# Performance work log

Measured on AMD Instinct MI355X. Metric: run time of the kernel, lower is better.

## Reference

```python
import jax, jax.numpy as jnp
import numpy as np

EPS = 1e-5
N_GROUPS = 32
N_HEAD = 1


def group_norm(x, gamma, beta):
    B, C, H, W = x.shape
    xg = x.reshape(B, N_GROUPS, C // N_GROUPS, H, W)
    mean = xg.mean(axis=(2, 3, 4), keepdims=True)
    var = xg.var(axis=(2, 3, 4), keepdims=True)
    xg = (xg - mean) * jax.lax.rsqrt(var + EPS)
    x = xg.reshape(B, C, H, W)
    return x * gamma[None, :, None, None] + beta[None, :, None, None]


def setup_inputs() -> dict:
    key = jax.random.key(0)
    k1, k2, k3 = jax.random.split(key, 3)
    B, C, H, W = 32, 512, 32, 32
    x = jax.random.normal(k1, (B, C, H, W), dtype=jnp.float32)
    gamma = jnp.ones((C,), dtype=jnp.float32)
    beta = jnp.zeros((C,), dtype=jnp.float32)
    # fan_avg uniform init for 1x1 convs (bound = sqrt(3*scale/fan_avg))
    bound_qkv = np.sqrt(3.0 / ((C + 3 * C) / 2))
    w_qkv = jax.random.uniform(k2, (3 * C, C), dtype=jnp.float32,
                               minval=-bound_qkv, maxval=bound_qkv)
    b_qkv = jnp.zeros((3 * C,), dtype=jnp.float32)
    bound_out = np.sqrt(3.0 * 1e-10 / C)
    w_out = jax.random.uniform(k3, (C, C), dtype=jnp.float32,
                               minval=-bound_out, maxval=bound_out)
    b_out = jnp.zeros((C,), dtype=jnp.float32)
    return {"x": x, "gamma": gamma, "beta": beta,
            "w_qkv": w_qkv, "b_qkv": b_qkv, "w_out": w_out, "b_out": b_out}


def reference(x, gamma, beta, w_qkv, b_qkv, w_out, b_out):
    B, C, H, W = x.shape
    n_head = N_HEAD
    head_dim = C // n_head
    norm = group_norm(x, gamma, beta)
    # 1x1 conv == channel matmul: [B,3C,H,W]
    qkv = jnp.einsum('bchw,oc->bohw', norm, w_qkv) + b_qkv[None, :, None, None]
    qkv = qkv.reshape(B, n_head, 3 * head_dim, H, W)
    q, k, v = jnp.split(qkv, 3, axis=2)  # each [B,n,hd,H,W]
    scale = 1.0 / np.sqrt(head_dim)
    attn = jnp.einsum('bnchw,bncyx->bnhwyx', q, k) * scale
    attn = jax.nn.softmax(attn.reshape(B, n_head, H, W, H * W), axis=-1)
    attn = attn.reshape(B, n_head, H, W, H, W)
    out = jnp.einsum('bnhwyx,bncyx->bnchw', attn, v).reshape(B, C, H, W)
    out = jnp.einsum('bchw,oc->bohw', out, w_out) + b_out[None, :, None, None]
    return out + x
```

## Files before the change

kernel.cpp:

```cpp
#include <hip/hip_runtime.h>
#include <hip/hip_bf16.h>

#define B_    32
#define C_    512
#define S_    1024
#define G_    32
#define CPG_  16
#define EPS_  1e-5f
#define SCALE_ 0.044194173824159216f

typedef __attribute__((ext_vector_type(4))) float  floatx4;
typedef __attribute__((ext_vector_type(8))) __bf16 bf16x8;

__device__ __forceinline__ float bf2f(unsigned short u) {
    union { unsigned int i; float f; } v; v.i = ((unsigned int)u) << 16; return v.f;
}
__device__ __forceinline__ unsigned short f2bf(float f) {
    union { float f; unsigned int i; } v; v.f = f;
    unsigned int r = v.i + 0x7fffu + ((v.i >> 16) & 1u);
    return (unsigned short)(r >> 16);
}

__device__ __forceinline__ void gl16(const unsigned short* g, unsigned short* l) {
    __builtin_amdgcn_global_load_lds(
        (const __attribute__((address_space(1))) unsigned int*)g,
        (__attribute__((address_space(3))) unsigned int*)l, 16, 0, 0);
}

__global__ __launch_bounds__(256) void gn_stats(const float* __restrict__ x,
                                                float2* __restrict__ stats,
                                                float* __restrict__ lbuf) {
    if (threadIdx.x < 8)
        ((float4*)lbuf)[blockIdx.x * 8 + threadIdx.x] = make_float4(0.f, 0.f, 0.f, 0.f);
    const size_t base = (size_t)blockIdx.x * (CPG_ * S_);
    const float4* xp = (const float4*)(x + base);
    float s = 0.f, ss = 0.f;
    for (int i = threadIdx.x; i < (CPG_ * S_) / 4; i += 256) {
        float4 v = xp[i];
        s  += v.x + v.y + v.z + v.w;
        ss += v.x * v.x + v.y * v.y + v.z * v.z + v.w * v.w;
    }
    #pragma unroll
    for (int o = 32; o; o >>= 1) { s += __shfl_down(s, o); ss += __shfl_down(ss, o); }
    __shared__ float a1[4], a2[4];
    const int wid = threadIdx.x >> 6, lane = threadIdx.x & 63;
    if (lane == 0) { a1[wid] = s; a2[wid] = ss; }
    __syncthreads();
    if (threadIdx.x == 0) {
        float S  = a1[0] + a1[1] + a1[2] + a1[3];
        float SS = a2[0] + a2[1] + a2[2] + a2[3];
        float mean = S * (1.f / 16384.f);
        float var  = SS * (1.f / 16384.f) - mean * mean;
        stats[blockIdx.x] = make_float2(mean, rsqrtf(var + EPS_));
    }
}

__global__ __launch_bounds__(256) void tcast(const float* __restrict__ w,
                                             const float* __restrict__ w_out,
                                             unsigned short* __restrict__ WqT,
                                             unsigned short* __restrict__ WkT,
                                             unsigned short* __restrict__ WvT,
                                             unsigned short* __restrict__ Woutb) {
    const int z = blockIdx.z;
    const int m0 = blockIdx.y * 64, c0 = blockIdx.x * 64;
    const int t = threadIdx.x, tr = t >> 4, tc4 = (t & 15) * 4;
    if (z == 3) {
        #pragma unroll
        for (int i = 0; i < 4; i++) {
            int r = tr + i * 16;
            float4 v = *(const float4*)(w_out + (size_t)(m0 + r) * 512 + c0 + tc4);
            ushort4 o4;
            o4.x = f2bf(v.x); o4.y = f2bf(v.y); o4.z = f2bf(v.z); o4.w = f2bf(v.w);
            *(ushort4*)(Woutb + (size_t)(m0 + r) * 512 + c0 + tc4) = o4;
        }
        return;
    }
    const float* src = w + (size_t)z * 262144;
    unsigned short* dst = (z == 0) ? WqT : (z == 1) ? WkT : WvT;
    __shared__ float tile[64][65];
    #pragma unroll
    for (int i = 0; i < 4; i++) {
        int r = tr + i * 16;
        float4 v = *(const float4*)(src + (size_t)(m0 + r) * 512 + c0 + tc4);
        tile[r][tc4 + 0] = v.x; tile[r][tc4 + 1] = v.y;
        tile[r][tc4 + 2] = v.z; tile[r][tc4 + 3] = v.w;
    }
    __syncthreads();
    #pragma unroll
    for (int i = 0; i < 4; i++) {
        int sr = tr + i * 16;
        ushort4 o4;
        o4.x = f2bf(tile[tc4 + 0][sr]); o4.y = f2bf(tile[tc4 + 1][sr]);
        o4.z = f2bf(tile[tc4 + 2][sr]); o4.w = f2bf(tile[tc4 + 3][sr]);
        *(ushort4*)(dst + (size_t)(c0 + sr) * 512 + m0 + tc4) = o4;
    }
}

__global__ __launch_bounds__(256) void vecprep(const unsigned short* __restrict__ WkT,
                                               const float* __restrict__ w_out,
                                               const float* __restrict__ b_qkv,
                                               float* __restrict__ bzv) {
    const int o = blockIdx.x, t = threadIdx.x;
    float us = 0.f, bv = 0.f;
    #pragma unroll
    for (int mm = 0; mm < 2; mm++) {
        int m = t + mm * 256;
        us += b_qkv[m] * bf2f(WkT[(size_t)o * 512 + m]);
        bv += w_out[(size_t)o * 512 + m] * b_qkv[1024 + m];
    }
    #pragma unroll
    for (int sh = 32; sh; sh >>= 1) { us += __shfl_down(us, sh); bv += __shfl_down(bv, sh); }
    __shared__ float a[2][4];
    const int wid = t >> 6, lane = t & 63;
    if (lane == 0) { a[0][wid] = us; a[1][wid] = bv; }
    __syncthreads();
    if (t == 0) {
        bzv[o]       = (a[0][0] + a[0][1] + a[0][2] + a[0][3]) * SCALE_;
        bzv[512 + o] =  a[1][0] + a[1][1] + a[1][2] + a[1][3];
    }
}

template<bool SWAP>
__device__ __forceinline__ void mfma_loop(const unsigned short* __restrict__ Ag, int lda,
                                          const unsigned short* __restrict__ Bg, int ldb,
                                          int K, int m0, int n0,
                                          unsigned short* ldsA, unsigned short* ldsB,
                                          floatx4 (&acc)[4][4]) {
    const int t = threadIdx.x, lane = t & 63, wave = t >> 6;
    const int wr = (wave >> 1) * 64, wc = (wave & 1) * 64;
    const int lrow = lane & 15, lq = lane >> 4;
    const int srow = wave * 16 + (lane >> 2);
    const int scol = (lane & 3) * 8;
    const unsigned short* gA0 = Ag + (size_t)(m0 + srow) * lda + scol;
    const unsigned short* gA1 = gA0 + (size_t)64 * lda;
    const unsigned short* gB0 = Bg + (size_t)(n0 + srow) * ldb + scol;
    const unsigned short* gB1 = gB0 + (size_t)64 * ldb;
    unsigned short* lA = ldsA + wave * 512;
    unsigned short* lB = ldsB + wave * 512;
    for (int k0 = 0; k0 < K; k0 += 64) {
        gl16(gA0 + k0,      lA);
        gl16(gA1 + k0,      lA + 2048);
        gl16(gA0 + k0 + 32, lA + 4096);
        gl16(gA1 + k0 + 32, lA + 6144);
        gl16(gB0 + k0,      lB);
        gl16(gB1 + k0,      lB + 2048);
        gl16(gB0 + k0 + 32, lB + 4096);
        gl16(gB1 + k0 + 32, lB + 6144);
        __syncthreads();
        #pragma unroll
        for (int sub = 0; sub < 2; sub++) {
            bf16x8 af[4], bfr[4];
            #pragma unroll
            for (int i = 0; i < 4; i++) {
                af[i]  = *(const bf16x8*)(ldsA + sub * 4096 + (wr + i * 16 + lrow) * 32 + lq * 8);
                bfr[i] = *(const bf16x8*)(ldsB + sub * 4096 + (wc + i * 16 + lrow) * 32 + lq * 8);
            }
            #pragma unroll
            for (int i = 0; i < 4; i++)
                #pragma unroll
                for (int j = 0; j < 4; j++) {
                    if (SWAP)
                        acc[i][j] = __builtin_amdgcn_mfma_f32_16x16x32_bf16(bfr[j], af[i], acc[i][j], 0, 0, 0);
                    else
                        acc[i][j] = __builtin_amdgcn_mfma_f32_16x16x32_bf16(af[i], bfr[j], acc[i][j], 0, 0, 0);
                }
        }
        __syncthreads();
    }
}

__global__ __launch_bounds__(256) void prep_gemm(const unsigned short* __restrict__ WkT,
                                                 const unsigned short* __restrict__ WqT,
                                                 const unsigned short* __restrict__ Woutb,
                                                 const unsigned short* __restrict__ WvT,
                                                 unsigned short* __restrict__ Wzv) {
    __shared__ __align__(16) unsigned short ldsA[2 * 128 * 32];
    __shared__ __align__(16) unsigned short ldsB[2 * 128 * 32];
    const int z = blockIdx.z;
    const int m0 = blockIdx.y * 128, n0 = blockIdx.x * 128;
    const int t = threadIdx.x, lane = t & 63, wave = t >> 6;
    const int wr = (wave >> 1) * 64, wc = (wave & 1) * 64;
    const int lrow = lane & 15, lq = lane >> 4;
    floatx4 acc[4][4];
    #pragma unroll
    for (int i = 0; i < 4; i++)
        #pragma unroll
        for (int j = 0; j < 4; j++) acc[i][j] = (floatx4){0.f, 0.f, 0.f, 0.f};
    const unsigned short* Ag = z ? Woutb : WkT;
    const unsigned short* Bg = z ? WvT   : WqT;
    mfma_loop<true>(Ag, 512, Bg, 512, 512, m0, n0, ldsA, ldsB, acc);
    const float sc = z ? 1.f : SCALE_;
    #pragma unroll
    for (int i = 0; i < 4; i++)
        #pragma unroll
        for (int j = 0; j < 4; j++) {
            int row = z * 512 + m0 + wr + i * 16 + lrow;
            int col = n0 + wc + j * 16 + lq * 4;
            floatx4 v = acc[i][j];
            ushort4 o4;
            o4.x = f2bf(v[0] * sc); o4.y = f2bf(v[1] * sc);
            o4.z = f2bf(v[2] * sc); o4.w = f2bf(v[3] * sc);
            *(ushort4*)(Wzv + (size_t)row * 512 + col) = o4;
        }
}

__global__ __launch_bounds__(256) void xnt_kernel(const float* __restrict__ x,
                                                  const float* __restrict__ gamma,
                                                  const float* __restrict__ beta,
                                                  const float2* __restrict__ stats,
                                                  unsigned short* __restrict__ xnt) {
    const int b = blockIdx.z, c0 = blockIdx.y * 64, s0 = blockIdx.x * 64;
    __shared__ float tile[64][65];
    const float* xb = x + (size_t)b * (C_ * S_);
    const int t = threadIdx.x, tr = t >> 4, tc4 = (t & 15) * 4;
    #pragma unroll
    for (int i = 0; i < 4; i++) {
        int r = tr + i * 16;
        int c = c0 + r;
        float2 mv = stats[b * G_ + (c >> 4)];
        float a  = mv.y * gamma[c];
        float bb = beta[c] - mv.x * a;
        float4 v = *(const float4*)(xb + (size_t)c * S_ + s0 + tc4);
        tile[r][tc4 + 0] = a * v.x + bb;
        tile[r][tc4 + 1] = a * v.y + bb;
        tile[r][tc4 + 2] = a * v.z + bb;
        tile[r][tc4 + 3] = a * v.w + bb;
    }
    __syncthreads();
    unsigned short* xo = xnt + (size_t)b * (S_ * C_);
    #pragma unroll
    for (int i = 0; i < 4; i++) {
        int sr = tr + i * 16;
        ushort4 o4;
        o4.x = f2bf(tile[tc4 + 0][sr]);
        o4.y = f2bf(tile[tc4 + 1][sr]);
        o4.z = f2bf(tile[tc4 + 2][sr]);
        o4.w = f2bf(tile[tc4 + 3][sr]);
        *(ushort4*)(xo + (size_t)(s0 + sr) * C_ + c0 + tc4) = o4;
    }
}

template<bool SWAP>
__device__ __forceinline__ void mfma256_loop(const unsigned short* __restrict__ Ag, int lda,
                                             const unsigned short* __restrict__ Bg, int ldb,
                                             int nt, int m0, int n0,
                                             unsigned short* lds, floatx4 (&acc)[8][4]) {
    const int tid  = threadIdx.x;
    const int lane = tid & 63, wave = tid >> 6;
    const int wm = wave >> 2, wn = wave & 3;
    const int lrow = lane & 15, lq = lane >> 4;
    const int cs = lq ^ ((lrow >> 1) & 3);

    int aofs[8], bofs[4];
    #pragma unroll
    for (int i = 0; i < 8; i++) aofs[i] = (wm * 128 + i * 16 + lrow) * 32 + cs * 8;
    #pragma unroll
    for (int j = 0; j < 4; j++) bofs[j] = (wn * 64 + j * 16 + lrow) * 32 + cs * 8;

    const int sr  = tid >> 2;
    const int scs = (tid & 3) ^ ((tid >> 3) & 3);
    const unsigned short* gA = Ag + (size_t)(m0 + sr) * lda + scs * 8;
    const unsigned short* gB = Bg + (size_t)(n0 + sr) * ldb + scs * 8;
    const size_t a128 = (size_t)128 * lda, b128 = (size_t)128 * ldb;
    unsigned short* lwA = lds + wave * 512;
    unsigned short* lwB = lds + 32768 + wave * 512;

#define STAGE_A(t, kh) do { \
    unsigned short* lb_ = lwA + ((t) & 1) * 16384 + (kh) * 8192; \
    const unsigned short* gp_ = gA + (t) * 64 + (kh) * 32; \
    gl16(gp_, lb_); gl16(gp_ + a128, lb_ + 4096); } while (0)
#define STAGE_B(t, kh) do { \
    unsigned short* lb_ = lwB + ((t) & 1) * 16384 + (kh) * 8192; \
    const unsigned short* gp_ = gB + (t) * 64 + (kh) * 32; \
    gl16(gp_, lb_); gl16(gp_ + b128, lb_ + 4096); } while (0)

    STAGE_A(0, 0); STAGE_B(0, 0); STAGE_A(0, 1); STAGE_B(0, 1);
    STAGE_A(1, 0); STAGE_B(1, 0);
    asm volatile("s_waitcnt vmcnt(4)" ::: "memory");
    __builtin_amdgcn_s_barrier();

    bf16x8 af[4], bfr[4];
    for (int u = 0; u < nt; ++u) {
        const int p = u & 1;
        #pragma unroll
        for (int ph = 0; ph < 4; ++ph) {
            const int kh = ph >> 1, mh = ph & 1;
            const int slab = p * 16384 + kh * 8192;
            if (mh == 0) {
                #pragma unroll
                for (int j = 0; j < 4; j++)
                    bfr[j] = *(const bf16x8*)(lds + 32768 + slab + bofs[j]);
            }
            #pragma unroll
            for (int i = 0; i < 4; i++)
                af[i] = *(const bf16x8*)(lds + slab + aofs[mh * 4 + i]);
            if (ph == 0)      { if (u + 1 < nt) STAGE_A(u + 1, 1); }
            else if (ph == 1) { if (u + 1 < nt) STAGE_B(u + 1, 1); }
            else if (ph == 2) { if (u + 2 < nt) STAGE_A(u + 2, 0); }
            else              { if (u + 2 < nt) STAGE_B(u + 2, 0); }
            __builtin_amdgcn_s_barrier();
            asm volatile("s_waitcnt lgkmcnt(0)" ::: "memory");
            __builtin_amdgcn_sched_barrier(0);
            __builtin_amdgcn_s_setprio(1);
            #pragma unroll
            for (int i = 0; i < 4; i++)
                #pragma unroll
                for (int j = 0; j < 4; j++) {
                    if (SWAP)
                        acc[mh * 4 + i][j] = __builtin_amdgcn_mfma_f32_16x16x32_bf16(
                            bfr[j], af[i], acc[mh * 4 + i][j], 0, 0, 0);
                    else
                        acc[mh * 4 + i][j] = __builtin_amdgcn_mfma_f32_16x16x32_bf16(
                            af[i], bfr[j], acc[mh * 4 + i][j], 0, 0, 0);
                }
            __builtin_amdgcn_s_setprio(0);
            if (ph < 3) {
                __builtin_amdgcn_s_barrier();
            } else if (u < nt - 2) {
                asm volatile("s_waitcnt vmcnt(4)" ::: "memory");
                __builtin_amdgcn_s_barrier();
            } else if (u == nt - 2) {
                asm volatile("s_waitcnt vmcnt(0)" ::: "memory");
                __builtin_amdgcn_s_barrier();
            }
        }
    }
#undef STAGE_A
#undef STAGE_B
}

#define GEMM256_VARS                                                  \
    __shared__ __align__(16) unsigned short lds[65536];               \
    const int lane = threadIdx.x & 63, wave = threadIdx.x >> 6;       \
    const int wm = wave >> 2, wn = wave & 3;                          \
    const int lrow = lane & 15, lq = lane >> 4;                       \
    floatx4 acc[8][4];                                                \
    _Pragma("unroll") for (int i = 0; i < 8; i++)                     \
        _Pragma("unroll") for (int j = 0; j < 4; j++)                 \
            acc[i][j] = (floatx4){0.f, 0.f, 0.f, 0.f};

__global__ __launch_bounds__(512, 2) void zv_mfma(const unsigned short* __restrict__ Wzv,
                                                  const unsigned short* __restrict__ xnt,
                                                  const float* __restrict__ bzv,
                                                  unsigned short* __restrict__ Zb,
                                                  unsigned short* __restrict__ Vb) {
    const int f = blockIdx.x;
    const int xcd = f & 7, j = f >> 3;
    const int b = xcd + 8 * (j >> 4);
    const int tile = j & 15;
    const int m0 = (tile >> 2) * 256, n0 = (tile & 3) * 256;
    GEMM256_VARS
    const unsigned short* Bg = xnt + (size_t)b * (S_ * C_);
    if (m0 < 512) {
        mfma256_loop<false>(Wzv, C_, Bg, C_, 8, m0, n0, lds, acc);
        unsigned short* dst = Zb + (size_t)b * (S_ * C_);
        #pragma unroll
        for (int i = 0; i < 8; i++)
            #pragma unroll
            for (int j2 = 0; j2 < 4; j2++) {
                int oabs = m0 + wm * 128 + i * 16 + lq * 4;
                int s    = n0 + wn * 64 + j2 * 16 + lrow;
                float4 bi = *(const float4*)(bzv + oabs);
                floatx4 v = acc[i][j2];
                ushort4 o4;
                o4.x = f2bf(v[0] + bi.x); o4.y = f2bf(v[1] + bi.y);
                o4.z = f2bf(v[2] + bi.z); o4.w = f2bf(v[3] + bi.w);
                *(ushort4*)(dst + (size_t)s * C_ + oabs) = o4;
            }
    } else {
        mfma256_loop<true>(Wzv, C_, Bg, C_, 8, m0, n0, lds, acc);
        unsigned short* dst = Vb + (size_t)b * (C_ * S_);
        #pragma unroll
        for (int i = 0; i < 8; i++)
            #pragma unroll
            for (int j2 = 0; j2 < 4; j2++) {
                int row = m0 + wm * 128 + i * 16 + lrow;
                int c   = row - 512;
                int sb  = n0 + wn * 64 + j2 * 16 + lq * 4;
                float bi = bzv[row];
                floatx4 v = acc[i][j2];
                ushort4 o4;
                o4.x = f2bf(v[0] + bi); o4.y = f2bf(v[1] + bi);
                o4.z = f2bf(v[2] + bi); o4.w = f2bf(v[3] + bi);
                *(ushort4*)(dst + (size_t)c * S_ + sb) = o4;
            }
    }
}

__global__ __launch_bounds__(512, 2) void scores_exp(const unsigned short* __restrict__ Zb,
                                                     const unsigned short* __restrict__ xnt,
                                                     unsigned short* __restrict__ Pb,
                                                     float* __restrict__ l) {
    const int f = blockIdx.x;
    const int xcd = f & 7, j = f >> 3;
    const int b = xcd + 8 * (j >> 4);
    const int tile = j & 15;
    const int m0 = (tile >> 2) * 256, n0 = (tile & 3) * 256;
    GEMM256_VARS
    const unsigned short* Ag = Zb  + (size_t)b * (S_ * C_);
    const unsigned short* Bg = xnt + (size_t)b * (S_ * C_);
    mfma256_loop<true>(Ag, C_, Bg, C_, 8, m0, n0, lds, acc);
    unsigned short* pp = Pb + (size_t)b * (S_ * S_);
    float* lb = l + b * S_;
    float rsv[8];
    #pragma unroll
    for (int i = 0; i < 8; i++) {
        int q = m0 + wm * 128 + i * 16 + lrow;
        float rs = 0.f;
        #pragma unroll
        for (int j2 = 0; j2 < 4; j2++) {
            int kv = n0 + wn * 64 + j2 * 16 + lq * 4;
            floatx4 v = acc[i][j2];
            float e0 = __expf(v[0]), e1 = __expf(v[1]);
            float e2 = __expf(v[2]), e3 = __expf(v[3]);
            rs += (e0 + e1) + (e2 + e3);
            ushort4 o4;
            o4.x = f2bf(e0); o4.y = f2bf(e1); o4.z = f2bf(e2); o4.w = f2bf(e3);
            *(ushort4*)(pp + (size_t)q * S_ + kv) = o4;
        }
        rs += __shfl_xor(rs, 16);
        rs += __shfl_xor(rs, 32);
        rsv[i] = rs;
    }
    __syncthreads();
    float* sred = (float*)lds;
    if (lane < 16) {
        #pragma unroll
        for (int i = 0; i < 8; i++)
            sred[wn * 256 + wm * 128 + i * 16 + lrow] = rsv[i];
    }
    __syncthreads();
    if (threadIdx.x < 256) {
        int q = threadIdx.x;
        float sum = (sred[q] + sred[256 + q]) + (sred[512 + q] + sred[768 + q]);
        atomicAdd(lb + m0 + q, sum);
    }
}

__global__ __launch_bounds__(512, 2) void pv_out(const unsigned short* __restrict__ Vb,
                                                 const unsigned short* __restrict__ Pb,
                                                 const float* __restrict__ l,
                                                 const float* __restrict__ bout,
                                                 const float* __restrict__ x,
                                                 float* __restrict__ out) {
    const int f = blockIdx.x;
    const int xcd = f & 7, j = f >> 3;
    const int b = xcd + 8 * (j >> 3);
    const int tile = j & 7;
    const int m0 = (tile & 1) * 256, n0 = (tile >> 1) * 256;
    GEMM256_VARS
    const unsigned short* Ag = Vb + (size_t)b * (C_ * S_);
    const unsigned short* Bg = Pb + (size_t)b * (S_ * S_);
    mfma256_loop<true>(Ag, S_, Bg, S_, 16, m0, n0, lds, acc);
    const float* lb = l + b * S_;
    const float* xb = x + (size_t)b * (C_ * S_);
    float* ob = out + (size_t)b * (C_ * S_);
    #pragma unroll
    for (int i = 0; i < 8; i++) {
        int c = m0 + wm * 128 + i * 16 + lrow;
        float bb = bout[c];
        #pragma unroll
        for (int j2 = 0; j2 < 4; j2++) {
            int s = n0 + wn * 64 + j2 * 16 + lq * 4;
            float4 lv = *(const float4*)(lb + s);
            size_t idx = (size_t)c * S_ + s;
            float4 xv = *(const float4*)(xb + idx);
            floatx4 v = acc[i][j2];
            float4 r;
            r.x = v[0] * __frcp_rn(lv.x) + bb + xv.x;
            r.y = v[1] * __frcp_rn(lv.y) + bb + xv.y;
            r.z = v[2] * __frcp_rn(lv.z) + bb + xv.z;
            r.w = v[3] * __frcp_rn(lv.w) + bb + xv.w;
            *(float4*)(ob + idx) = r;
        }
    }
}

extern "C" void kernel_launch(void* const* d_in, const int* in_sizes, int n_in,
                              void* d_out, int out_size, void* d_ws, size_t ws_size,
                              hipStream_t stream) {
    const float* x      = (const float*)d_in[0];
    const float* gamma  = (const float*)d_in[1];
    const float* beta   = (const float*)d_in[2];
    const float* w_qkv  = (const float*)d_in[3];
    const float* b_qkv  = (const float*)d_in[4];
    const float* w_out  = (const float*)d_in[5];
    const float* b_out  = (const float*)d_in[6];
    float* out          = (float*)d_out;

    char* ws = (char*)d_ws;
    unsigned short* Zb    = (unsigned short*)(ws);
    unsigned short* Vb    = (unsigned short*)(ws + 33554432ULL);
    unsigned short* xnt   = (unsigned short*)(ws + 67108864ULL);
    unsigned short* Pb    = (unsigned short*)(ws + 100663296ULL);
    unsigned short* WqT   = (unsigned short*)(ws + 167772160ULL);
    unsigned short* WkT   = (unsigned short*)(ws + 167772160ULL + 524288ULL);
    unsigned short* WvT   = (unsigned short*)(ws + 167772160ULL + 1048576ULL);
    unsigned short* Woutb = (unsigned short*)(ws + 167772160ULL + 1572864ULL);
    unsigned short* Wzv   = (unsigned short*)(ws + 167772160ULL + 2097152ULL);
    float*          bzv   = (float*)(ws + 167772160ULL + 3145728ULL);
    float2*         stats = (float2*)(ws + 167772160ULL + 3153920ULL);
    float*          lbuf  = (float*)(ws + 167772160ULL + 3162112ULL);

    gn_stats <<<B_ * G_, 256, 0, stream>>>(x, stats, lbuf);
    tcast    <<<dim3(8, 8, 4), 256, 0, stream>>>(w_qkv, w_out, WqT, WkT, WvT, Woutb);
    prep_gemm<<<dim3(4, 4, 2), 256, 0, stream>>>(WkT, WqT, Woutb, WvT, Wzv);
    vecprep  <<<512, 256, 0, stream>>>(WkT, w_out, b_qkv, bzv);
    xnt_kernel<<<dim3(16, 8, B_), 256, 0, stream>>>(x, gamma, beta, stats, xnt);
    zv_mfma  <<<512, 512, 0, stream>>>(Wzv, xnt, bzv, Zb, Vb);
    scores_exp<<<512, 512, 0, stream>>>(Zb, xnt, Pb, lbuf);
    pv_out   <<<256, 512, 0, stream>>>(Vb, Pb, lbuf, b_out, x, out);
}
```

Baseline: 306.5 us.

## Shrink GEMM tiles to 256x128 with single-stage K=32 pipeline and higher occupancy

Replaces the 256x256 block tile, which used a double-buffered four-phase K=64 pipeline, with a 256x128 tile (8 waves in a 4x2 layout, 64x64 per wave). Each K=32 step is staged once, with a full vmcnt(0) wait and a barrier every iteration. The smaller tile cuts LDS and accumulator registers, so launch bounds rise to 4 blocks per CU and grid sizes double, aiming at better occupancy and load balance. The cost is lower data reuse per block, twice the global traffic for the shared operand, and less latency hiding, since each step now waits for all of its loads to finish.

```diff
diff --git a/kernel.cpp b/kernel.cpp
--- a/kernel.cpp
+++ b/kernel.cpp
@@ -241,124 +241,94 @@
 }
 
 template<bool SWAP>
-__device__ __forceinline__ void mfma256_loop(const unsigned short* __restrict__ Ag, int lda,
+__device__ __forceinline__ void mfma128_loop(const unsigned short* __restrict__ Ag, int lda,
                                              const unsigned short* __restrict__ Bg, int ldb,
                                              int nt, int m0, int n0,
-                                             unsigned short* lds, floatx4 (&acc)[8][4]) {
-    const int tid  = threadIdx.x;
-    const int lane = tid & 63, wave = tid >> 6;
-    const int wm = wave >> 2, wn = wave & 3;
+                                             unsigned short* lds, floatx4 (&acc)[4][4]) {
+    const int tid = threadIdx.x, lane = tid & 63, wave = tid >> 6;
+    const int wm = wave >> 1, wn = wave & 1;
     const int lrow = lane & 15, lq = lane >> 4;
     const int cs = lq ^ ((lrow >> 1) & 3);
-
-    int aofs[8], bofs[4];
-    #pragma unroll
-    for (int i = 0; i < 8; i++) aofs[i] = (wm * 128 + i * 16 + lrow) * 32 + cs * 8;
-    #pragma unroll
-    for (int j = 0; j < 4; j++) bofs[j] = (wn * 64 + j * 16 + lrow) * 32 + cs * 8;
+    const int aob = (wm * 64 + lrow) * 32 + cs * 8;
+    const int bob = 16384 + (wn * 64 + lrow) * 32 + cs * 8;
 
     const int sr  = tid >> 2;
     const int scs = (tid & 3) ^ ((tid >> 3) & 3);
     const unsigned short* gA = Ag + (size_t)(m0 + sr) * lda + scs * 8;
     const unsigned short* gB = Bg + (size_t)(n0 + sr) * ldb + scs * 8;
-    const size_t a128 = (size_t)128 * lda, b128 = (size_t)128 * ldb;
+    const size_t a128 = (size_t)128 * lda;
     unsigned short* lwA = lds + wave * 512;
-    unsigned short* lwB = lds + 32768 + wave * 512;
-
-#define STAGE_A(t, kh) do { \
-    unsigned short* lb_ = lwA + ((t) & 1) * 16384 + (kh) * 8192; \
-    const unsigned short* gp_ = gA + (t) * 64 + (kh) * 32; \
-    gl16(gp_, lb_); gl16(gp_ + a128, lb_ + 4096); } while (0)
-#define STAGE_B(t, kh) do { \
-    unsigned short* lb_ = lwB + ((t) & 1) * 16384 + (kh) * 8192; \
-    const unsigned short* gp_ = gB + (t) * 64 + (kh) * 32; \
-    gl16(gp_, lb_); gl16(gp_ + b128, lb_ + 4096); } while (0)
-
-    STAGE_A(0, 0); STAGE_B(0, 0); STAGE_A(0, 1); STAGE_B(0, 1);
-    STAGE_A(1, 0); STAGE_B(1, 0);
-    asm volatile("s_waitcnt vmcnt(4)" ::: "memory");
+    unsigned short* lwB = lds + 16384 + wave * 512;
+
+#define STG(t) do { \
+    unsigned short* la_ = lwA + ((t) & 1) * 8192; \
+    gl16(gA + (t) * 32,        la_); \
+    gl16(gA + (t) * 32 + a128, la_ + 4096); \
+    gl16(gB + (t) * 32,        lwB + ((t) & 1) * 4096); } while (0)
+
+    STG(0);
+    asm volatile("s_waitcnt vmcnt(0)" ::: "memory");
     __builtin_amdgcn_s_barrier();
 
-    bf16x8 af[4], bfr[4];
     for (int u = 0; u < nt; ++u) {
-        const int p = u & 1;
-        #pragma unroll
-        for (int ph = 0; ph < 4; ++ph) {
-            const int kh = ph >> 1, mh = ph & 1;
-            const int slab = p * 16384 + kh * 8192;
-            if (mh == 0) {
-                #pragma unroll
-                for (int j = 0; j < 4; j++)
-                    bfr[j] = *(const bf16x8*)(lds + 32768 + slab + bofs[j]);
+        const int pa = (u & 1) * 8192, pb = (u & 1) * 4096;
+        bf16x8 af[4], bfr[4];
+        #pragma unroll
+        for (int j = 0; j < 4; j++) bfr[j] = *(const bf16x8*)(lds + pb + bob + j * 512);
+        #pragma unroll
+        for (int i = 0; i < 4; i++) af[i]  = *(const bf16x8*)(lds + pa + aob + i * 512);
+        if (u + 1 < nt) STG(u + 1);
+        asm volatile("s_waitcnt lgkmcnt(0)" ::: "memory");
+        __builtin_amdgcn_sched_barrier(0);
+        __builtin_amdgcn_s_setprio(1);
+        #pragma unroll
+        for (int i = 0; i < 4; i++)
+            #pragma unroll
+            for (int j = 0; j < 4; j++) {
+                if (SWAP)
+                    acc[i][j] = __builtin_amdgcn_mfma_f32_16x16x32_bf16(
+                        bfr[j], af[i], acc[i][j], 0, 0, 0);
+                else
+                    acc[i][j] = __builtin_amdgcn_mfma_f32_16x16x32_bf16(
+                        af[i], bfr[j], acc[i][j], 0, 0, 0);
             }
-            #pragma unroll
-            for (int i = 0; i < 4; i++)
-                af[i] = *(const bf16x8*)(lds + slab + aofs[mh * 4 + i]);
-            if (ph == 0)      { if (u + 1 < nt) STAGE_A(u + 1, 1); }
-            else if (ph == 1) { if (u + 1 < nt) STAGE_B(u + 1, 1); }
-            else if (ph == 2) { if (u + 2 < nt) STAGE_A(u + 2, 0); }
-            else              { if (u + 2 < nt) STAGE_B(u + 2, 0); }
-            __builtin_amdgcn_s_barrier();
-            asm volatile("s_waitcnt lgkmcnt(0)" ::: "memory");
-            __builtin_amdgcn_sched_barrier(0);
-            __builtin_amdgcn_s_setprio(1);
-            #pragma unroll
-            for (int i = 0; i < 4; i++)
-                #pragma unroll
-                for (int j = 0; j < 4; j++) {
-                    if (SWAP)
-                        acc[mh * 4 + i][j] = __builtin_amdgcn_mfma_f32_16x16x32_bf16(
-                            bfr[j], af[i], acc[mh * 4 + i][j], 0, 0, 0);
-                    else
-                        acc[mh * 4 + i][j] = __builtin_amdgcn_mfma_f32_16x16x32_bf16(
-                            af[i], bfr[j], acc[mh * 4 + i][j], 0, 0, 0);
-                }
-            __builtin_amdgcn_s_setprio(0);
-            if (ph < 3) {
-                __builtin_amdgcn_s_barrier();
-            } else if (u < nt - 2) {
-                asm volatile("s_waitcnt vmcnt(4)" ::: "memory");
-                __builtin_amdgcn_s_barrier();
-            } else if (u == nt - 2) {
-                asm volatile("s_waitcnt vmcnt(0)" ::: "memory");
-                __builtin_amdgcn_s_barrier();
-            }
-        }
-    }
-#undef STAGE_A
-#undef STAGE_B
-}
-
-#define GEMM256_VARS                                                  \
-    __shared__ __align__(16) unsigned short lds[65536];               \
+        __builtin_amdgcn_s_setprio(0);
+        asm volatile("s_waitcnt vmcnt(0)" ::: "memory");
+        __builtin_amdgcn_s_barrier();
+    }
+#undef STG
+}
+
+#define GEMM128_VARS                                                  \
+    __shared__ __align__(16) unsigned short lds[24576];               \
     const int lane = threadIdx.x & 63, wave = threadIdx.x >> 6;       \
-    const int wm = wave >> 2, wn = wave & 3;                          \
+    const int wm = wave >> 1, wn = wave & 1;                          \
     const int lrow = lane & 15, lq = lane >> 4;                       \
-    floatx4 acc[8][4];                                                \
-    _Pragma("unroll") for (int i = 0; i < 8; i++)                     \
+    floatx4 acc[4][4];                                                \
+    _Pragma("unroll") for (int i = 0; i < 4; i++)                     \
         _Pragma("unroll") for (int j = 0; j < 4; j++)                 \
             acc[i][j] = (floatx4){0.f, 0.f, 0.f, 0.f};
 
-__global__ __launch_bounds__(512, 2) void zv_mfma(const unsigned short* __restrict__ Wzv,
+__global__ __launch_bounds__(512, 4) void zv_mfma(const unsigned short* __restrict__ Wzv,
                                                   const unsigned short* __restrict__ xnt,
                                                   const float* __restrict__ bzv,
                                                   unsigned short* __restrict__ Zb,
                                                   unsigned short* __restrict__ Vb) {
     const int f = blockIdx.x;
     const int xcd = f & 7, j = f >> 3;
-    const int b = xcd + 8 * (j >> 4);
-    const int tile = j & 15;
-    const int m0 = (tile >> 2) * 256, n0 = (tile & 3) * 256;
-    GEMM256_VARS
+    const int b = xcd + 8 * (j >> 5);
+    const int tile = j & 31;
+    const int m0 = (tile >> 3) * 256, n0 = (tile & 7) * 128;
+    GEMM128_VARS
     const unsigned short* Bg = xnt + (size_t)b * (S_ * C_);
     if (m0 < 512) {
-        mfma256_loop<false>(Wzv, C_, Bg, C_, 8, m0, n0, lds, acc);
+        mfma128_loop<false>(Wzv, C_, Bg, C_, 16, m0, n0, lds, acc);
         unsigned short* dst = Zb + (size_t)b * (S_ * C_);
         #pragma unroll
-        for (int i = 0; i < 8; i++)
+        for (int i = 0; i < 4; i++)
             #pragma unroll
             for (int j2 = 0; j2 < 4; j2++) {
-                int oabs = m0 + wm * 128 + i * 16 + lq * 4;
+                int oabs = m0 + wm * 64 + i * 16 + lq * 4;
                 int s    = n0 + wn * 64 + j2 * 16 + lrow;
                 float4 bi = *(const float4*)(bzv + oabs);
                 floatx4 v = acc[i][j2];
@@ -368,13 +338,13 @@
                 *(ushort4*)(dst + (size_t)s * C_ + oabs) = o4;
             }
     } else {
-        mfma256_loop<true>(Wzv, C_, Bg, C_, 8, m0, n0, lds, acc);
+        mfma128_loop<true>(Wzv, C_, Bg, C_, 16, m0, n0, lds, acc);
         unsigned short* dst = Vb + (size_t)b * (C_ * S_);
         #pragma unroll
-        for (int i = 0; i < 8; i++)
+        for (int i = 0; i < 4; i++)
             #pragma unroll
             for (int j2 = 0; j2 < 4; j2++) {
-                int row = m0 + wm * 128 + i * 16 + lrow;
+                int row = m0 + wm * 64 + i * 16 + lrow;
                 int c   = row - 512;
                 int sb  = n0 + wn * 64 + j2 * 16 + lq * 4;
                 float bi = bzv[row];
@@ -387,25 +357,25 @@
     }
 }
 
-__global__ __launch_bounds__(512, 2) void scores_exp(const unsigned short* __restrict__ Zb,
+__global__ __launch_bounds__(512, 4) void scores_exp(const unsigned short* __restrict__ Zb,
                                                      const unsigned short* __restrict__ xnt,
                                                      unsigned short* __restrict__ Pb,
                                                      float* __restrict__ l) {
     const int f = blockIdx.x;
     const int xcd = f & 7, j = f >> 3;
-    const int b = xcd + 8 * (j >> 4);
-    const int tile = j & 15;
-    const int m0 = (tile >> 2) * 256, n0 = (tile & 3) * 256;
-    GEMM256_VARS
+    const int b = xcd + 8 * (j >> 5);
+    const int tile = j & 31;
+    const int m0 = (tile >> 3) * 256, n0 = (tile & 7) * 128;
+    GEMM128_VARS
     const unsigned short* Ag = Zb  + (size_t)b * (S_ * C_);
     const unsigned short* Bg = xnt + (size_t)b * (S_ * C_);
-    mfma256_loop<true>(Ag, C_, Bg, C_, 8, m0, n0, lds, acc);
+    mfma128_loop<true>(Ag, C_, Bg, C_, 16, m0, n0, lds, acc);
     unsigned short* pp = Pb + (size_t)b * (S_ * S_);
     float* lb = l + b * S_;
-    float rsv[8];
-    #pragma unroll
-    for (int i = 0; i < 8; i++) {
-        int q = m0 + wm * 128 + i * 16 + lrow;
+    float rsv[4];
+    #pragma unroll
+    for (int i = 0; i < 4; i++) {
+        int q = m0 + wm * 64 + i * 16 + lrow;
         float rs = 0.f;
         #pragma unroll
         for (int j2 = 0; j2 < 4; j2++) {
@@ -426,18 +396,17 @@
     float* sred = (float*)lds;
     if (lane < 16) {
         #pragma unroll
-        for (int i = 0; i < 8; i++)
-            sred[wn * 256 + wm * 128 + i * 16 + lrow] = rsv[i];
+        for (int i = 0; i < 4; i++)
+            sred[wn * 256 + wm * 64 + i * 16 + lrow] = rsv[i];
     }
     __syncthreads();
     if (threadIdx.x < 256) {
         int q = threadIdx.x;
-        float sum = (sred[q] + sred[256 + q]) + (sred[512 + q] + sred[768 + q]);
-        atomicAdd(lb + m0 + q, sum);
-    }
-}
-
-__global__ __launch_bounds__(512, 2) void pv_out(const unsigned short* __restrict__ Vb,
+        atomicAdd(lb + m0 + q, sred[q] + sred[256 + q]);
+    }
+}
+
+__global__ __launch_bounds__(512, 4) void pv_out(const unsigned short* __restrict__ Vb,
                                                  const unsigned short* __restrict__ Pb,
                                                  const float* __restrict__ l,
                                                  const float* __restrict__ bout,
@@ -445,19 +414,19 @@
                                                  float* __restrict__ out) {
     const int f = blockIdx.x;
     const int xcd = f & 7, j = f >> 3;
-    const int b = xcd + 8 * (j >> 3);
-    const int tile = j & 7;
-    const int m0 = (tile & 1) * 256, n0 = (tile >> 1) * 256;
-    GEMM256_VARS
+    const int b = xcd + 8 * (j >> 4);
+    const int tile = j & 15;
+    const int m0 = (tile >> 3) * 256, n0 = (tile & 7) * 128;
+    GEMM128_VARS
     const unsigned short* Ag = Vb + (size_t)b * (C_ * S_);
     const unsigned short* Bg = Pb + (size_t)b * (S_ * S_);
-    mfma256_loop<true>(Ag, S_, Bg, S_, 16, m0, n0, lds, acc);
+    mfma128_loop<true>(Ag, S_, Bg, S_, 32, m0, n0, lds, acc);
     const float* lb = l + b * S_;
     const float* xb = x + (size_t)b * (C_ * S_);
     float* ob = out + (size_t)b * (C_ * S_);
     #pragma unroll
-    for (int i = 0; i < 8; i++) {
-        int c = m0 + wm * 128 + i * 16 + lrow;
+    for (int i = 0; i < 4; i++) {
+        int c = m0 + wm * 64 + i * 16 + lrow;
         float bb = bout[c];
         #pragma unroll
         for (int j2 = 0; j2 < 4; j2++) {
@@ -507,7 +476,7 @@
     prep_gemm<<<dim3(4, 4, 2), 256, 0, stream>>>(WkT, WqT, Woutb, WvT, Wzv);
     vecprep  <<<512, 256, 0, stream>>>(WkT, w_out, b_qkv, bzv);
     xnt_kernel<<<dim3(16, 8, B_), 256, 0, stream>>>(x, gamma, beta, stats, xnt);
-    zv_mfma  <<<512, 512, 0, stream>>>(Wzv, xnt, bzv, Zb, Vb);
-    scores_exp<<<512, 512, 0, stream>>>(Zb, xnt, Pb, lbuf);
-    pv_out   <<<256, 512, 0, stream>>>(Vb, Pb, lbuf, b_out, x, out);
-}
+    zv_mfma  <<<1024, 512, 0, stream>>>(Wzv, xnt, bzv, Zb, Vb);
+    scores_exp<<<1024, 512, 0, stream>>>(Zb, xnt, Pb, lbuf);
+    pv_out   <<<512, 512, 0, stream>>>(Vb, Pb, lbuf, b_out, x, out);
+}
```

New measurement: 315.9 us. 3.1% more time.
